# Kernel optimization log

Measured on AMD Instinct MI355X. Metric: run time of the kernel, lower is better.

## Reference

```python
import jax, jax.numpy as jnp
import numpy as np

B, DIN, H = 16384, 512, 512
K = 7  # LC_i1, LC_i2, LC_f1, LC_f2, LC_o, LC_z (gate nets, idx 0..5), LC_d (decay net, idx 6)


def setup_inputs() -> dict:
    key = jax.random.key(0)
    ks = jax.random.split(key, 8)
    s1 = 1.0 / np.sqrt(DIN)
    s2 = 1.0 / np.sqrt(H)
    return {
        "hx": jax.random.normal(ks[0], (B, DIN), jnp.float32),
        "cx1": jax.random.normal(ks[1], (B, H), jnp.float32),
        "cx2": jax.random.normal(ks[2], (B, H), jnp.float32),
        # stacked params for the 7 sub-networks (same structure: Linear(DIN,H) -> Linear(H,H))
        "W1": jax.random.uniform(ks[3], (K, H, DIN), jnp.float32, -s1, s1),
        "b1": jax.random.uniform(ks[4], (K, H), jnp.float32, -s1, s1),
        "W2": jax.random.uniform(ks[5], (K, H, H), jnp.float32, -s2, s2),
        "b2": jax.random.uniform(ks[6], (K, H), jnp.float32, -s2, s2),
    }


def reference(hx, cx1, cx2, W1, b1, W2, b2):
    # layer 1 for all 7 nets at once: [K, B, H]
    h1 = jnp.einsum('bd,khd->kbh', hx, W1) + b1[:, None, :]
    # gate nets use tanh, decay net uses softplus
    a1 = jnp.concatenate([jnp.tanh(h1[:6]), jax.nn.softplus(h1[6:])], axis=0)
    # layer 2: [K, B, H]
    h2 = jnp.einsum('kbh,kgh->kbg', a1, W2) + b2[:, None, :]
    gates = jax.nn.sigmoid(jnp.tanh(h2[:6]))  # Gate_network: sigmoid(tanh(.))
    d = jax.nn.softplus(h2[6])                # Decay_network output (decay_coef, side state)
    i1, i2, f1, f2, o, zg = gates
    z = jnp.tanh(zg)                          # z = Tanh(LC_z(hx))
    cy1 = f1 * cx1 + i1 * z                   # side state self.cy1
    cy2 = f2 * cx2 + i2 * z
    return cy2
```

## Files before the change

### kernel.cpp

```cpp
#include <hip/hip_runtime.h>
#include <hip/hip_bf16.h>

typedef __attribute__((ext_vector_type(8))) __bf16 bf16x8;
typedef __attribute__((ext_vector_type(4))) __bf16 bf16x4;
typedef __attribute__((ext_vector_type(4))) float f32x4;

constexpr int M = 16384;
constexpr int K = 512;
constexpr int BK = 32;

__device__ __forceinline__ void async_copy16(const void* gsrc, void* ldst) {
  __builtin_amdgcn_global_load_lds(
      (const __attribute__((address_space(1))) unsigned int*)(gsrc),
      (__attribute__((address_space(3))) unsigned int*)(ldst),
      16, 0, 0);
}

__device__ __forceinline__ float frcp(float x) { return __builtin_amdgcn_rcpf(x); }
__device__ __forceinline__ float ftanh(float x) {
  return 1.0f - 2.0f * frcp(1.0f + __expf(2.0f * x));
}
__device__ __forceinline__ float fsigm(float x) { return frcp(1.0f + __expf(-x)); }

template <int MODE>
__global__ __launch_bounds__(256) void gemm_kernel(
    const float* __restrict__ hx,
    const __bf16* __restrict__ Ab,
    const __bf16* __restrict__ W,
    const float* __restrict__ bias,
    __bf16* __restrict__ outb,
    const __bf16* __restrict__ gates,
    const float* __restrict__ cx2,
    float* __restrict__ outf)
{
  const int j = blockIdx.z;
  const int jj = (MODE == 3) ? 2 : j;
  const int mbase = blockIdx.x * 128;
  const int nbase = blockIdx.y * 128;
  constexpr size_t NH = (size_t)M * 512;

  const __bf16* Wj = W + (size_t)jj * 262144;
  const __bf16* Abj = (MODE >= 2) ? Ab + (size_t)jj * NH : nullptr;
  const int brow = 2 * jj + 1;

  __shared__ __align__(16) __bf16 smem[17408];

  const int tid  = threadIdx.x;
  const int wid  = tid >> 6;
  const int lane = tid & 63;
  const int wm   = (wid >> 1) * 64;
  const int wn   = (wid & 1) * 64;
  const int srow = wid * 16 + (lane >> 2);
  const int scol = ((lane & 3) ^ ((lane >> 3) & 3)) * 8;
  const int fr   = lane & 15;
  const int kc   = lane >> 4;
  const int sw   = (fr >> 1) & 3;
  const int rowq = kc * 4;

  const int ar = tid >> 1;
  const int cb = (tid & 1) * 2;
  const int asw = (ar >> 1) & 3;
  const float* hxrow =
      (MODE == 1) ? hx + (size_t)(mbase + ar) * K + cb * 8 : nullptr;

  auto stage = [&](int p, int k0) {
    __bf16* As = smem + p * 8192;
    __bf16* Bs = As + 4096;
#pragma unroll
    for (int r = 0; r < 2; ++r)
      async_copy16(Wj + (size_t)(nbase + r * 64 + srow) * K + (k0 + scol),
                   (void*)&Bs[(r * 64 + wid * 16) * BK]);
    if constexpr (MODE >= 2) {
#pragma unroll
      for (int r = 0; r < 2; ++r)
        async_copy16(Abj + (size_t)(mbase + r * 64 + srow) * K + (k0 + scol),
                     (void*)&As[(r * 64 + wid * 16) * BK]);
    } else {
      const float* hp = hxrow + k0;
      f32x4 v0 = *(const f32x4*)(hp);
      f32x4 v1 = *(const f32x4*)(hp + 4);
      f32x4 v2 = *(const f32x4*)(hp + 8);
      f32x4 v3 = *(const f32x4*)(hp + 12);
      __bf16* As_ = As + ar * 32;
      *(bf16x4*)&As_[(cb ^ asw) * 8]           = __builtin_convertvector(v0, bf16x4);
      *(bf16x4*)&As_[(cb ^ asw) * 8 + 4]       = __builtin_convertvector(v1, bf16x4);
      *(bf16x4*)&As_[((cb + 1) ^ asw) * 8]     = __builtin_convertvector(v2, bf16x4);
      *(bf16x4*)&As_[((cb + 1) ^ asw) * 8 + 4] = __builtin_convertvector(v3, bf16x4);
    }
  };

  f32x4 acc[4][4] = {};

  stage(0, 0);
  int p = 0;
  for (int k0 = 0; k0 < K; k0 += BK) {
    __syncthreads();
    if (k0 + BK < K) stage(p ^ 1, k0 + BK);

    const __bf16* As = smem + p * 8192;
    const __bf16* Bs = As + 4096;
    bf16x8 af[4], bfr[4];
#pragma unroll
    for (int i = 0; i < 4; ++i) {
      af[i]  = *(const bf16x8*)&As[(wm + i * 16 + fr) * BK + ((kc ^ sw) * 8)];
      bfr[i] = *(const bf16x8*)&Bs[(wn + i * 16 + fr) * BK + ((kc ^ sw) * 8)];
    }
#pragma unroll
    for (int mi = 0; mi < 4; ++mi)
#pragma unroll
      for (int ni = 0; ni < 4; ++ni)
        acc[mi][ni] = __builtin_amdgcn_mfma_f32_16x16x32_bf16(
            af[mi], bfr[ni], acc[mi][ni], 0, 0, 0);
    p ^= 1;
  }

  float bv[4];
  const float* bj = bias + (size_t)brow * 512 + nbase + wn;
#pragma unroll
  for (int ni = 0; ni < 4; ++ni) bv[ni] = bj[ni * 16 + fr];

  if constexpr (MODE <= 2) {
    __syncthreads();
#pragma unroll
    for (int mi = 0; mi < 4; ++mi)
#pragma unroll
      for (int ni = 0; ni < 4; ++ni)
#pragma unroll
        for (int r = 0; r < 4; ++r) {
          float v = acc[mi][ni][r] + bv[ni];
          float res = (MODE == 1) ? ftanh(v) : fsigm(ftanh(v));
          smem[(wm + mi * 16 + rowq + r) * 136 + (wn + ni * 16 + fr)] =
              (__bf16)res;
        }
    __syncthreads();
#pragma unroll
    for (int it = 0; it < 8; ++it) {
      const int s = it * 256 + tid;
      const int row = s >> 4, ch = s & 15;
      bf16x8 v = *(const bf16x8*)&smem[row * 136 + ch * 8];
      *(bf16x8*)&outb[(size_t)j * NH + (size_t)(mbase + row) * 512 +
                      (nbase + ch * 8)] = v;
    }
  } else {
#pragma unroll
    for (int mi = 0; mi < 4; ++mi)
#pragma unroll
      for (int ni = 0; ni < 4; ++ni)
#pragma unroll
        for (int r = 0; r < 4; ++r) {
          float v = acc[mi][ni][r] + bv[ni];
          const __bf16 zb = (__bf16)ftanh(fsigm(ftanh(v)));
          const size_t idx =
              (size_t)(mbase + wm + mi * 16 + rowq + r) * 512 +
              (nbase + wn + ni * 16 + fr);
          outf[idx] = (float)gates[NH + idx] * cx2[idx] +
                      (float)gates[idx] * (float)zb;
        }
  }
}

__global__ __launch_bounds__(256) void cvt_w6(const float* __restrict__ W1,
                                              const float* __restrict__ W2,
                                              __bf16* __restrict__ dst) {
  const int y = blockIdx.y;
  const float* src = (y < 3) ? W1 + (size_t)(2 * y + 1) * 262144
                             : W2 + (size_t)(2 * (y - 3) + 1) * 262144;
  __bf16* d = dst + (size_t)y * 262144;
  const size_t i = ((size_t)blockIdx.x * 256 + threadIdx.x) * 4;
  f32x4 v = *(const f32x4*)&src[i];
  *(bf16x4*)&d[i] = __builtin_convertvector(v, bf16x4);
}

extern "C" void kernel_launch(void* const* d_in, const int* in_sizes, int n_in,
                              void* d_out, int out_size, void* d_ws, size_t ws_size,
                              hipStream_t stream) {
  const float* hx  = (const float*)d_in[0];
  const float* cx2 = (const float*)d_in[2];
  const float* W1  = (const float*)d_in[3];
  const float* b1  = (const float*)d_in[4];
  const float* W2  = (const float*)d_in[5];
  const float* b2  = (const float*)d_in[6];
  float* out = (float*)d_out;

  char* ws = (char*)d_ws;
  __bf16* W1b   = (__bf16*)(ws);
  __bf16* W2b   = (__bf16*)(ws + 1572864);
  __bf16* a1    = (__bf16*)(ws + 3145728);
  __bf16* gates = (__bf16*)(ws + 53477376);

  cvt_w6<<<dim3(256, 6), 256, 0, stream>>>(W1, W2, W1b);

  gemm_kernel<1><<<dim3(128, 4, 3), 256, 0, stream>>>(
      hx, nullptr, W1b, b1, a1, nullptr, nullptr, nullptr);
  gemm_kernel<2><<<dim3(128, 4, 2), 256, 0, stream>>>(
      nullptr, a1, W2b, b2, gates, nullptr, nullptr, nullptr);
  gemm_kernel<3><<<dim3(128, 4, 1), 256, 0, stream>>>(
      nullptr, a1, W2b, b2, nullptr, gates, cx2, out);
}
```

Measured before the change: 271.5 us.

## Prefetch hx into registers and vectorize epilogue via swizzled LDS staging

The layer-1 GEMM now issues the global fp32 loads of hx for the next k-tile before the MFMA loop and writes them to LDS afterwards, so load latency overlaps compute. The epilogue staging buffer uses an XOR swizzle instead of padding, which cuts LDS size. The final GEMM stages its activations through LDS so it can read gates and cx2 and write the output with 16-byte vector accesses instead of scattered scalar ones. This adds register pressure for the held hx values and an extra LDS round trip in the final kernel.

```diff
diff --git a/kernel.cpp b/kernel.cpp
--- a/kernel.cpp
+++ b/kernel.cpp
@@ -21,6 +21,10 @@
   return 1.0f - 2.0f * frcp(1.0f + __expf(2.0f * x));
 }
 __device__ __forceinline__ float fsigm(float x) { return frcp(1.0f + __expf(-x)); }
+
+__device__ __forceinline__ int kswz(int row) {
+  return ((row & 3) << 3) ^ ((row & 12) << 2);
+}
 
 template <int MODE>
 __global__ __launch_bounds__(256) void gemm_kernel(
@@ -43,7 +47,7 @@
   const __bf16* Abj = (MODE >= 2) ? Ab + (size_t)jj * NH : nullptr;
   const int brow = 2 * jj + 1;
 
-  __shared__ __align__(16) __bf16 smem[17408];
+  __shared__ __align__(16) __bf16 smem[16384];
 
   const int tid  = threadIdx.x;
   const int wid  = tid >> 6;
@@ -63,7 +67,7 @@
   const float* hxrow =
       (MODE == 1) ? hx + (size_t)(mbase + ar) * K + cb * 8 : nullptr;
 
-  auto stage = [&](int p, int k0) {
+  auto stageW = [&](int p, int k0) {
     __bf16* As = smem + p * 8192;
     __bf16* Bs = As + 4096;
 #pragma unroll
@@ -75,27 +79,43 @@
       for (int r = 0; r < 2; ++r)
         async_copy16(Abj + (size_t)(mbase + r * 64 + srow) * K + (k0 + scol),
                      (void*)&As[(r * 64 + wid * 16) * BK]);
-    } else {
-      const float* hp = hxrow + k0;
-      f32x4 v0 = *(const f32x4*)(hp);
-      f32x4 v1 = *(const f32x4*)(hp + 4);
-      f32x4 v2 = *(const f32x4*)(hp + 8);
-      f32x4 v3 = *(const f32x4*)(hp + 12);
-      __bf16* As_ = As + ar * 32;
-      *(bf16x4*)&As_[(cb ^ asw) * 8]           = __builtin_convertvector(v0, bf16x4);
-      *(bf16x4*)&As_[(cb ^ asw) * 8 + 4]       = __builtin_convertvector(v1, bf16x4);
-      *(bf16x4*)&As_[((cb + 1) ^ asw) * 8]     = __builtin_convertvector(v2, bf16x4);
-      *(bf16x4*)&As_[((cb + 1) ^ asw) * 8 + 4] = __builtin_convertvector(v3, bf16x4);
     }
   };
 
+  f32x4 av0, av1, av2, av3;
+  auto loadA = [&](int k0) {
+    const float* hp = hxrow + k0;
+    av0 = *(const f32x4*)(hp);
+    av1 = *(const f32x4*)(hp + 4);
+    av2 = *(const f32x4*)(hp + 8);
+    av3 = *(const f32x4*)(hp + 12);
+  };
+  auto writeA = [&](int p) {
+    __bf16* As_ = smem + p * 8192 + ar * 32;
+    *(bf16x4*)&As_[(cb ^ asw) * 8]           = __builtin_convertvector(av0, bf16x4);
+    *(bf16x4*)&As_[(cb ^ asw) * 8 + 4]       = __builtin_convertvector(av1, bf16x4);
+    *(bf16x4*)&As_[((cb + 1) ^ asw) * 8]     = __builtin_convertvector(av2, bf16x4);
+    *(bf16x4*)&As_[((cb + 1) ^ asw) * 8 + 4] = __builtin_convertvector(av3, bf16x4);
+  };
+
   f32x4 acc[4][4] = {};
 
-  stage(0, 0);
+  if constexpr (MODE == 1) {
+    loadA(0);
+    stageW(0, 0);
+    writeA(0);
+  } else {
+    stageW(0, 0);
+  }
+
   int p = 0;
   for (int k0 = 0; k0 < K; k0 += BK) {
     __syncthreads();
-    if (k0 + BK < K) stage(p ^ 1, k0 + BK);
+    const bool pre = k0 + BK < K;
+    if (pre) {
+      if constexpr (MODE == 1) loadA(k0 + BK);
+      stageW(p ^ 1, k0 + BK);
+    }
 
     const __bf16* As = smem + p * 8192;
     const __bf16* Bs = As + 4096;
@@ -111,6 +131,9 @@
       for (int ni = 0; ni < 4; ++ni)
         acc[mi][ni] = __builtin_amdgcn_mfma_f32_16x16x32_bf16(
             af[mi], bfr[ni], acc[mi][ni], 0, 0, 0);
+
+    if constexpr (MODE == 1)
+      if (pre) writeA(p ^ 1);
     p ^= 1;
   }
 
@@ -119,43 +142,53 @@
 #pragma unroll
   for (int ni = 0; ni < 4; ++ni) bv[ni] = bj[ni * 16 + fr];
 
+  __syncthreads();
+#pragma unroll
+  for (int mi = 0; mi < 4; ++mi)
+#pragma unroll
+    for (int ni = 0; ni < 4; ++ni)
+#pragma unroll
+      for (int r = 0; r < 4; ++r) {
+        float v = acc[mi][ni][r] + bv[ni];
+        float res;
+        if constexpr (MODE == 1) res = ftanh(v);
+        else if constexpr (MODE == 2) res = fsigm(ftanh(v));
+        else res = ftanh(fsigm(ftanh(v)));
+        const int row = wm + mi * 16 + rowq + r;
+        const int col = wn + ni * 16 + fr;
+        smem[row * 128 + (col ^ kswz(row))] = (__bf16)res;
+      }
+  __syncthreads();
+
   if constexpr (MODE <= 2) {
-    __syncthreads();
-#pragma unroll
-    for (int mi = 0; mi < 4; ++mi)
-#pragma unroll
-      for (int ni = 0; ni < 4; ++ni)
-#pragma unroll
-        for (int r = 0; r < 4; ++r) {
-          float v = acc[mi][ni][r] + bv[ni];
-          float res = (MODE == 1) ? ftanh(v) : fsigm(ftanh(v));
-          smem[(wm + mi * 16 + rowq + r) * 136 + (wn + ni * 16 + fr)] =
-              (__bf16)res;
-        }
-    __syncthreads();
 #pragma unroll
     for (int it = 0; it < 8; ++it) {
       const int s = it * 256 + tid;
       const int row = s >> 4, ch = s & 15;
-      bf16x8 v = *(const bf16x8*)&smem[row * 136 + ch * 8];
+      bf16x8 v = *(const bf16x8*)&smem[row * 128 + ((ch * 8) ^ kswz(row))];
       *(bf16x8*)&outb[(size_t)j * NH + (size_t)(mbase + row) * 512 +
                       (nbase + ch * 8)] = v;
     }
   } else {
 #pragma unroll
-    for (int mi = 0; mi < 4; ++mi)
-#pragma unroll
-      for (int ni = 0; ni < 4; ++ni)
-#pragma unroll
-        for (int r = 0; r < 4; ++r) {
-          float v = acc[mi][ni][r] + bv[ni];
-          const __bf16 zb = (__bf16)ftanh(fsigm(ftanh(v)));
-          const size_t idx =
-              (size_t)(mbase + wm + mi * 16 + rowq + r) * 512 +
-              (nbase + wn + ni * 16 + fr);
-          outf[idx] = (float)gates[NH + idx] * cx2[idx] +
-                      (float)gates[idx] * (float)zb;
-        }
+    for (int it = 0; it < 8; ++it) {
+      const int s = it * 256 + tid;
+      const int row = s >> 4, ch = s & 15;
+      const size_t gidx = (size_t)(mbase + row) * 512 + (nbase + ch * 8);
+      bf16x8 zv = *(const bf16x8*)&smem[row * 128 + ((ch * 8) ^ kswz(row))];
+      bf16x8 i2 = *(const bf16x8*)&gates[gidx];
+      bf16x8 f2 = *(const bf16x8*)&gates[NH + gidx];
+      f32x4 c0 = *(const f32x4*)&cx2[gidx];
+      f32x4 c1 = *(const f32x4*)&cx2[gidx + 4];
+      f32x4 r0, r1;
+#pragma unroll
+      for (int q = 0; q < 4; ++q) {
+        r0[q] = (float)f2[q] * c0[q] + (float)i2[q] * (float)zv[q];
+        r1[q] = (float)f2[4 + q] * c1[q] + (float)i2[4 + q] * (float)zv[4 + q];
+      }
+      *(f32x4*)&outf[gidx] = r0;
+      *(f32x4*)&outf[gidx + 4] = r1;
+    }
   }
 }
 
```

Result: faster. 236.6 us (-12.8%).
